# Optimization experiments

Measured on AMD Instinct MI355X. Metric: run time of the kernel, lower is better.

Reference implementation:

```python
import jax, jax.numpy as jnp
import numpy as np

EPS = 1e-12
LAMBDA = 0.5  # kernel['lambda'] for the binary kernel

D, H, Z = 3072, 1024, 32
BS, NN = 128, 32


def setup_inputs() -> dict:
    key = jax.random.key(0)
    ks = jax.random.split(key, 16)
    sc = lambda fan_in: 1.0 / np.sqrt(fan_in)
    inp = {
        "x_c": jax.random.normal(ks[0], (BS, D), jnp.float32),
        "x_nn": jax.random.normal(ks[1], (BS, NN, D), jnp.float32),
        # encoder params: D -> H -> H -> Z
        "We1": jax.random.normal(ks[2], (D, H), jnp.float32) * sc(D),
        "be1": jnp.zeros((H,), jnp.float32),
        "We2": jax.random.normal(ks[3], (H, H), jnp.float32) * sc(H),
        "be2": jnp.zeros((H,), jnp.float32),
        "We3": jax.random.normal(ks[4], (H, Z), jnp.float32) * sc(H),
        "be3": jnp.zeros((Z,), jnp.float32),
        # decoder params: Z -> H -> H -> D
        "Wd1": jax.random.normal(ks[5], (Z, H), jnp.float32) * sc(Z),
        "bd1": jnp.zeros((H,), jnp.float32),
        "Wd2": jax.random.normal(ks[6], (H, H), jnp.float32) * sc(H),
        "bd2": jnp.zeros((H,), jnp.float32),
        "Wd3": jax.random.normal(ks[7], (H, D), jnp.float32) * sc(H),
        "bd3": jnp.zeros((D,), jnp.float32),
    }
    return inp


def _mlp(x, W1, b1, W2, b2, W3, b3):
    h = jax.nn.relu(x @ W1 + b1)
    h = jax.nn.relu(h @ W2 + b2)
    return h @ W3 + b3


def reference(x_c, x_nn, We1, be1, We2, be2, We3, be3,
              Wd1, bd1, Wd2, bd2, Wd3, bd3):
    bs, num_nn, dim = x_nn.shape

    enc = lambda x: _mlp(x, We1, be1, We2, be2, We3, be3)
    dec = lambda z: _mlp(z, Wd1, bd1, Wd2, bd2, Wd3, bd3)

    z_c = enc(x_c)                                   # (bs, Z)
    z_dim = z_c.shape[1]
    z_nn = enc(x_nn.reshape(-1, dim)).reshape(bs, num_nn, z_dim)

    recon = dec(z_c)                                 # (bs, D)
    dz = z_nn - z_c[:, None, :]                      # (bs, nn, Z)
    v = dz.reshape(-1, z_dim)                        # (bs*nn, Z)
    inputs = jnp.broadcast_to(z_c[:, None, :], (bs, num_nn, z_dim)).reshape(-1, z_dim)

    # approx_order == 2: Jacobian-vector and Hessian-bilinear (dz^T H dz) via nested jvp
    jac_fn = lambda z: jax.jvp(dec, (z,), (v,))[1]   # J(z) dz, (bs*nn, D)
    jac, hess = jax.jvp(jac_fn, (inputs,), (v,))     # each (bs*nn, D)

    n_recon = recon[:, None, :] + (jac + 0.5 * hess).reshape(bs, num_nn, dim)

    n_loss = jnp.sum((x_nn - n_recon) ** 2, axis=2)  # ||.||^2, (bs, nn)

    # binary kernel: 1 where neighbor differs from center, lambda where identical
    dist = jnp.linalg.norm(x_c[:, None, :] - x_nn, axis=2)
    weights = jnp.where(dist > EPS, 1.0, LAMBDA)

    loss = jnp.mean(weights * n_loss)
    return loss
```

## Files before the change

### kernel.cpp

```cpp
#include <hip/hip_runtime.h>
#include <math.h>

#define D_DIM 3072
#define H_DIM 1024
#define Z_DIM 32
#define BATCH 128
#define NNEI 32
#define NROWS (BATCH * NNEI)
#define MENC (NROWS + BATCH)

typedef __attribute__((ext_vector_type(8))) short short8;
typedef __attribute__((ext_vector_type(4))) float f32x4;
typedef unsigned short ushortT;

__device__ __forceinline__ unsigned short f2bf(float f) {
  union { float f; unsigned int u; } v; v.f = f;
  unsigned int r = v.u + 0x7FFFu + ((v.u >> 16) & 1u);
  return (unsigned short)(r >> 16);
}
__device__ __forceinline__ float bf2f(unsigned short b) {
  union { unsigned int u; float f; } v; v.u = ((unsigned int)b) << 16;
  return v.f;
}

__device__ __forceinline__ void gl16(const ushortT* g, ushortT* l) {
  typedef __attribute__((address_space(1))) const void gvoid;
  typedef __attribute__((address_space(3))) void lvoid;
  __builtin_amdgcn_global_load_lds((gvoid*)(const void*)g, (lvoid*)(void*)l,
                                   16, 0, 0);
}
#define BAR() asm volatile("s_barrier" ::: "memory")
#define VM0() asm volatile("s_waitcnt vmcnt(0)" ::: "memory")

template <int N>
__device__ __forceinline__ void vmw() {
  if constexpr (N == 0)      asm volatile("s_waitcnt vmcnt(0)" ::: "memory");
  else if constexpr (N == 2) asm volatile("s_waitcnt vmcnt(2)" ::: "memory");
  else if constexpr (N == 3) asm volatile("s_waitcnt vmcnt(3)" ::: "memory");
  else if constexpr (N == 4) asm volatile("s_waitcnt vmcnt(4)" ::: "memory");
  else if constexpr (N == 6) asm volatile("s_waitcnt vmcnt(6)" ::: "memory");
  else if constexpr (N == 8) asm volatile("s_waitcnt vmcnt(8)" ::: "memory");
}

enum { EP_RELU = 0, EP_BIAS = 1, EP_PART = 2, EP_LOSS = 3 };

template <int MODE, int TN>
__global__ __launch_bounds__(256) __attribute__((amdgpu_waves_per_eu(2)))
void gemm32(
    const ushortT* __restrict__ A, const ushortT* __restrict__ BT,
    const float* __restrict__ bias, ushortT* __restrict__ C,
    float* __restrict__ P, int M, int N, int K, int Ks,
    const ushortT* __restrict__ xa,
    const float* __restrict__ wrow,
    float* __restrict__ out) {
  constexpr int NF = TN / 32;

  __shared__ __align__(16) ushortT As[4][4096];
  __shared__ __align__(16) ushortT Bs[4][TN * 32];

  const int t = threadIdx.x;
  const int wave = t >> 6;
  const int lane = t & 63;
  const int quad = lane >> 4;
  const int lm = lane & 15;

  int id = blockIdx.y * gridDim.x + blockIdx.x;
  const int nwg = gridDim.x * gridDim.y;
  if ((nwg & 7) == 0) id = (id & 7) * (nwg >> 3) + (id >> 3);
  const int bm = (id / gridDim.x) * 128;
  const int bn = (id % gridDim.x) * TN;

  const int koff = blockIdx.z * Ks;
  const int wr = (wave >> 1) * 64;
  const int wc = (wave & 1) * (TN / 2);

  f32x4 acc[4][NF];
#pragma unroll
  for (int i = 0; i < 4; ++i)
#pragma unroll
    for (int j = 0; j < NF; ++j) acc[i][j] = (f32x4)0.f;

  const int srow = lane & 15;
  const int skq = lane >> 4;
  const ushortT* gA =
      A + (size_t)(bm + wave * 32 + srow) * K + koff + skq * 8;
  const size_t row16 = (size_t)16 * K;

  const ushortT* gB;
  if (TN == 128) {
    gB = BT + (size_t)(bn + wave * 32 + srow) * K + koff + skq * 8;
  } else if (TN == 64) {
    gB = BT + (size_t)(bn + wave * 16 + srow) * K + koff + skq * 8;
  } else {
    gB = BT + (size_t)(bn + (wave & 1) * 16 + srow) * K + koff + skq * 8;
  }

#define STAGE(kk, sl)                                           \
  {                                                             \
    const size_t o = (size_t)(kk) * 32;                         \
    ushortT* lA = &As[sl][wave * 1024];                         \
    gl16(gA + o, lA);                                           \
    gl16(gA + row16 + o, lA + 512);                             \
    if (TN == 128) {                                            \
      ushortT* lB = &Bs[sl][wave * 1024];                       \
      gl16(gB + o, lB);                                         \
      gl16(gB + row16 + o, lB + 512);                           \
    } else if (TN == 64) {                                      \
      gl16(gB + o, &Bs[sl][wave * 512]);                        \
    } else {                                                    \
      if (wave < 2) gl16(gB + o, &Bs[sl][(wave & 1) * 512]);    \
    }                                                           \
  }

  const int nk = Ks / 32;
  for (int p = 0; p < 3 && p < nk; ++p) STAGE(p, p);

  for (int t0 = 0; t0 < nk; ++t0) {
    const int sl = t0 & 3;
    const int ahead = nk - 1 - t0;
    const int a2 = ahead >= 2 ? 2 : ahead;
    if (TN == 128) {
      if (a2 == 2) vmw<8>(); else if (a2 == 1) vmw<4>(); else vmw<0>();
    } else if (TN == 64) {
      if (a2 == 2) vmw<6>(); else if (a2 == 1) vmw<3>(); else vmw<0>();
    } else {
      if (wave < 2) {
        if (a2 == 2) vmw<6>(); else if (a2 == 1) vmw<3>(); else vmw<0>();
      } else {
        if (a2 == 2) vmw<4>(); else if (a2 == 1) vmw<2>(); else vmw<0>();
      }
    }
    BAR();
    if (t0 + 3 < nk) STAGE(t0 + 3, (t0 + 3) & 3);

    const ushortT* arp = &As[sl][(wr >> 4) * 512 + lane * 8];
    const ushortT* brp = &Bs[sl][(wc >> 4) * 512 + lane * 8];
    short8 af[4], bf[NF];
#pragma unroll
    for (int mt = 0; mt < 4; ++mt) af[mt] = *(const short8*)(arp + mt * 512);
#pragma unroll
    for (int nt = 0; nt < NF; ++nt) bf[nt] = *(const short8*)(brp + nt * 512);
#pragma unroll
    for (int mt = 0; mt < 4; ++mt)
#pragma unroll
      for (int nt = 0; nt < NF; ++nt)
        acc[mt][nt] = __builtin_amdgcn_mfma_f32_16x16x32_bf16(
            af[mt], bf[nt], acc[mt][nt], 0, 0, 0);
  }
#undef STAGE

  if (MODE == EP_LOSS) {
    __shared__ float red[256];
    float lsum = 0.f;
#pragma unroll
    for (int mt = 0; mt < 4; ++mt) {
#pragma unroll
      for (int r = 0; r < 4; ++r) {
        const int row = bm + wr + mt * 16 + quad * 4 + r;
        const float w = wrow[row];
        const ushortT* xr = xa + (size_t)row * N;
        float rs = 0.f;
#pragma unroll
        for (int nt = 0; nt < NF; ++nt) {
          const int col = bn + wc + nt * 16 + lm;
          const float d = bf2f(xr[col]) - (acc[mt][nt][r] + bias[col]);
          rs = fmaf(d, d, rs);
        }
        lsum = fmaf(w, rs, lsum);
      }
    }
    __syncthreads();
    red[t] = lsum;
    __syncthreads();
    for (int st = 128; st > 0; st >>= 1) {
      if (t < st) red[t] += red[t + st];
      __syncthreads();
    }
    if (t == 0) atomicAdd(out, red[0] * (1.0f / (float)NROWS));
  } else if (MODE == EP_PART) {
#pragma unroll
    for (int mt = 0; mt < 4; ++mt)
#pragma unroll
      for (int r = 0; r < 4; ++r) {
        const int row = bm + wr + mt * 16 + quad * 4 + r;
#pragma unroll
        for (int nt = 0; nt < NF; ++nt) {
          const int col = bn + wc + nt * 16 + lm;
          P[((size_t)blockIdx.z * M + row) * N + col] = acc[mt][nt][r];
        }
      }
  } else {
#pragma unroll
    for (int mt = 0; mt < 4; ++mt)
#pragma unroll
      for (int r = 0; r < 4; ++r) {
        const int row = bm + wr + mt * 16 + quad * 4 + r;
#pragma unroll
        for (int nt = 0; nt < NF; ++nt) {
          const int col = bn + wc + nt * 16 + lm;
          float v = acc[mt][nt][r] + bias[col];
          if (MODE == EP_RELU) v = fmaxf(v, 0.f);
          C[(size_t)row * N + col] = f2bf(v);
        }
      }
  }
}

template <int MODE, int TN>
__global__ __launch_bounds__(256) void gemm_sb(
    const ushortT* __restrict__ A, const ushortT* __restrict__ BT,
    const float* __restrict__ bias, ushortT* __restrict__ C,
    int M, int N, int K,
    const ushortT* __restrict__ xa, const float* __restrict__ wrow,
    float* __restrict__ out) {
  constexpr int NF = TN / 32;
  __shared__ __align__(16) ushortT As[4096];
  __shared__ __align__(16) ushortT Bs[TN * 32];

  const int t = threadIdx.x;
  const int wave = t >> 6;
  const int lane = t & 63;
  const int quad = lane >> 4;
  const int lm = lane & 15;

  int id = blockIdx.y * gridDim.x + blockIdx.x;
  const int nwg = gridDim.x * gridDim.y;
  if ((nwg & 7) == 0) id = (id & 7) * (nwg >> 3) + (id >> 3);
  const int bm = (id / gridDim.x) * 128;
  const int bn = (id % gridDim.x) * TN;

  const int wr = (wave >> 1) * 64;
  const int wc = (wave & 1) * (TN / 2);

  const int a_r0 = (t >> 6) * 16 + (t & 15);
  const int a_q8 = ((t >> 4) & 3) * 8;
  const ushortT* ga0 = A + (size_t)(bm + a_r0) * K + a_q8;
  const ushortT* gb0 = BT + (size_t)(bn + a_r0) * K + a_q8;

  ushortT* asw = &As[wave * 512];
  ushortT* bsw = &Bs[wave * 512];
  gl16(ga0, asw);
  gl16(ga0 + (size_t)64 * K, asw + 2048);
  gl16(gb0, bsw);
  if (TN == 128) gl16(gb0 + (size_t)64 * K, bsw + 2048);
  VM0();
  BAR();

  f32x4 acc[4][NF];
#pragma unroll
  for (int i = 0; i < 4; ++i)
#pragma unroll
    for (int j = 0; j < NF; ++j) acc[i][j] = (f32x4)0.f;

  const ushortT* arp = As + (wr >> 4) * 512 + lane * 8;
  const ushortT* brp = Bs + (wc >> 4) * 512 + lane * 8;
  short8 af[4], bf[NF];
#pragma unroll
  for (int mt = 0; mt < 4; ++mt) af[mt] = *(const short8*)(arp + mt * 512);
#pragma unroll
  for (int nt = 0; nt < NF; ++nt) bf[nt] = *(const short8*)(brp + nt * 512);
#pragma unroll
  for (int mt = 0; mt < 4; ++mt)
#pragma unroll
    for (int nt = 0; nt < NF; ++nt)
      acc[mt][nt] = __builtin_amdgcn_mfma_f32_16x16x32_bf16(
          af[mt], bf[nt], acc[mt][nt], 0, 0, 0);

#pragma unroll
  for (int mt = 0; mt < 4; ++mt)
#pragma unroll
    for (int r = 0; r < 4; ++r) {
      const int row = bm + wr + mt * 16 + quad * 4 + r;
#pragma unroll
      for (int nt = 0; nt < NF; ++nt) {
        const int col = bn + wc + nt * 16 + lm;
        float v = acc[mt][nt][r] + bias[col];
        if (MODE == EP_RELU) v = fmaxf(v, 0.f);
        C[(size_t)row * N + col] = f2bf(v);
      }
    }
}

template <int S, int RELU>
__global__ __launch_bounds__(256) void reduce_lin(
    const float* __restrict__ P, const float* __restrict__ bias,
    ushortT* __restrict__ outp, int MN, int Nmask) {
  const int i4 = (blockIdx.x * 256 + threadIdx.x) * 4;
  if (i4 >= MN) return;
  float4 s = *(const float4*)(P + i4);
#pragma unroll
  for (int k = 1; k < S; ++k) {
    const float4 q = *(const float4*)(P + (size_t)k * MN + i4);
    s.x += q.x; s.y += q.y; s.z += q.z; s.w += q.w;
  }
  const float4 b = *(const float4*)(bias + (i4 & Nmask));
  float vx = s.x + b.x, vy = s.y + b.y, vz = s.z + b.z, vw = s.w + b.w;
  if (RELU) {
    vx = fmaxf(vx, 0.f); vy = fmaxf(vy, 0.f);
    vz = fmaxf(vz, 0.f); vw = fmaxf(vw, 0.f);
  }
  ushort4 o;
  o.x = f2bf(vx); o.y = f2bf(vy); o.z = f2bf(vz); o.w = f2bf(vw);
  *(ushort4*)(outp + i4) = o;
}

__global__ __launch_bounds__(256) void mask_apply(
    const ushortT* __restrict__ U, ushortT* __restrict__ outp) {
  const int i4 = (blockIdx.x * 256 + threadIdx.x) * 4;
  const int r = i4 >> 10;
  const int c = i4 & 1023;
  ushort4 u = *(const ushort4*)(U + i4);
  ushort4 o;
  if (r < NROWS) {
    const ushort4 m = *(const ushort4*)(U + (((size_t)(NROWS + (r >> 5))) << 10) + c);
    o.x = ((short)m.x > 0) ? u.x : 0;
    o.y = ((short)m.y > 0) ? u.y : 0;
    o.z = ((short)m.z > 0) ? u.z : 0;
    o.w = ((short)m.w > 0) ? u.w : 0;
  } else {
    o.x = ((short)u.x > 0) ? u.x : 0;
    o.y = ((short)u.y > 0) ? u.y : 0;
    o.z = ((short)u.z > 0) ? u.z : 0;
    o.w = ((short)u.w > 0) ? u.w : 0;
  }
  *(ushort4*)(outp + i4) = o;
}

__global__ __launch_bounds__(256) void prep_kernel(
    const float* __restrict__ x_c, const float* __restrict__ x_nn,
    ushortT* __restrict__ A_enc, float* __restrict__ wbuf, float* __restrict__ out) {
  const int i = blockIdx.x;
  const int t = threadIdx.x;
  if (i < NROWS) {
    const float* src = x_nn + (size_t)i * D_DIM;
    const float* ctr = x_c + (size_t)(i >> 5) * D_DIM;
    ushortT* dst = A_enc + (size_t)i * D_DIM;
    float s = 0.f;
    for (int d = t * 4; d < D_DIM; d += 1024) {
      const float4 v = *(const float4*)(src + d);
      const float4 c = *(const float4*)(ctr + d);
      ushort4 o;
      o.x = f2bf(v.x); o.y = f2bf(v.y); o.z = f2bf(v.z); o.w = f2bf(v.w);
      *(ushort4*)(dst + d) = o;
      const float dx = v.x - c.x, dy = v.y - c.y, dz = v.z - c.z, dw = v.w - c.w;
      s += dx * dx + dy * dy + dz * dz + dw * dw;
    }
    __shared__ float red[256];
    red[t] = s;
    __syncthreads();
    for (int st = 128; st > 0; st >>= 1) {
      if (t < st) red[t] += red[t + st];
      __syncthreads();
    }
    if (t == 0) {
      wbuf[i] = (red[0] > 1e-24f) ? 1.0f : 0.5f;
      if (i == 0) out[0] = 0.f;
    }
  } else {
    const int r = i - NROWS;
    const float* src = x_c + (size_t)r * D_DIM;
    ushortT* dst = A_enc + (size_t)i * D_DIM;
    for (int d = t * 4; d < D_DIM; d += 1024) {
      const float4 v = *(const float4*)(src + d);
      ushort4 o;
      o.x = f2bf(v.x); o.y = f2bf(v.y); o.z = f2bf(v.z); o.w = f2bf(v.w);
      *(ushort4*)(dst + d) = o;
    }
  }
}

__global__ __launch_bounds__(256) void trans_all(
    const float* __restrict__ We1, const float* __restrict__ We2,
    const float* __restrict__ We3, const float* __restrict__ Wd1,
    const float* __restrict__ Wd2, const float* __restrict__ Wd3,
    ushortT* __restrict__ We1T, ushortT* __restrict__ We2T,
    ushortT* __restrict__ We3T, ushortT* __restrict__ Wd1T,
    ushortT* __restrict__ Wd2T, ushortT* __restrict__ Wd3T) {
  const int b = blockIdx.x;
  const float* W; ushortT* WT; int K, N, loc;
  if (b < 3072)      { W = We1; WT = We1T; K = 3072; N = 1024; loc = b; }
  else if (b < 4096) { W = We2; WT = We2T; K = 1024; N = 1024; loc = b - 3072; }
  else if (b < 4128) { W = We3; WT = We3T; K = 1024; N = 32;   loc = b - 4096; }
  else if (b < 4160) { W = Wd1; WT = Wd1T; K = 32;   N = 1024; loc = b - 4128; }
  else if (b < 5184) { W = Wd2; WT = Wd2T; K = 1024; N = 1024; loc = b - 4160; }
  else               { W = Wd3; WT = Wd3T; K = 1024; N = 3072; loc = b - 5184; }
  const int ntiles = N >> 5;
  const int n0 = (loc % ntiles) * 32;
  const int k0 = (loc / ntiles) * 32;
  __shared__ float tile[32][33];
  const int tx = threadIdx.x & 31;
  const int ty = threadIdx.x >> 5;
  for (int i = ty; i < 32; i += 8)
    tile[i][tx] = W[(size_t)(k0 + i) * N + n0 + tx];
  __syncthreads();
  for (int i = ty; i < 32; i += 8)
    WT[(size_t)(n0 + i) * K + k0 + tx] = f2bf(tile[tx][i]);
}

extern "C" void kernel_launch(void* const* d_in, const int* in_sizes, int n_in,
                              void* d_out, int out_size, void* d_ws, size_t ws_size,
                              hipStream_t stream) {
  const float* x_c = (const float*)d_in[0];
  const float* x_nn = (const float*)d_in[1];
  const float* We1 = (const float*)d_in[2];
  const float* be1 = (const float*)d_in[3];
  const float* We2 = (const float*)d_in[4];
  const float* be2 = (const float*)d_in[5];
  const float* We3 = (const float*)d_in[6];
  const float* be3 = (const float*)d_in[7];
  const float* Wd1 = (const float*)d_in[8];
  const float* bd1 = (const float*)d_in[9];
  const float* Wd2 = (const float*)d_in[10];
  const float* bd2 = (const float*)d_in[11];
  const float* Wd3 = (const float*)d_in[12];
  const float* bd3 = (const float*)d_in[13];
  float* out = (float*)d_out;

  char* p = (char*)d_ws;
  auto alloc = [&](size_t bytes) {
    char* r = p;
    p += (bytes + 255) & ~(size_t)255;
    return r;
  };
  ushortT* We1T = (ushortT*)alloc((size_t)H_DIM * D_DIM * 2);
  ushortT* We2T = (ushortT*)alloc((size_t)H_DIM * H_DIM * 2);
  ushortT* We3T = (ushortT*)alloc((size_t)Z_DIM * H_DIM * 2);
  ushortT* Wd1T = (ushortT*)alloc((size_t)H_DIM * Z_DIM * 2);
  ushortT* Wd2T = (ushortT*)alloc((size_t)H_DIM * H_DIM * 2);
  ushortT* Wd3T = (ushortT*)alloc((size_t)D_DIM * H_DIM * 2);
  ushortT* A_enc = (ushortT*)alloc((size_t)MENC * D_DIM * 2);
  ushortT* bufX = (ushortT*)alloc((size_t)MENC * H_DIM * 2);
  ushortT* bufY = (ushortT*)alloc((size_t)MENC * H_DIM * 2);
  ushortT* z = (ushortT*)alloc((size_t)MENC * Z_DIM * 2);
  float* Pbig = (float*)alloc((size_t)3 * MENC * H_DIM * 4);
  float* wbuf = (float*)alloc((size_t)NROWS * 4);

  const dim3 blk(256);
  const float* nofp = nullptr;
  const ushortT* nobf = nullptr;

  prep_kernel<<<dim3(MENC), blk, 0, stream>>>(x_c, x_nn, A_enc, wbuf, out);
  trans_all<<<dim3(8256), blk, 0, stream>>>(We1, We2, We3, Wd1, Wd2, Wd3,
                                            We1T, We2T, We3T, Wd1T, Wd2T, Wd3T);

  gemm32<EP_PART, 128><<<dim3(8, 33, 3), blk, 0, stream>>>(
      A_enc, We1T, nofp, nullptr, Pbig, MENC, H_DIM, D_DIM, D_DIM / 3,
      nobf, nofp, nullptr);
  reduce_lin<3, 1><<<dim3((MENC * H_DIM) / 1024), blk, 0, stream>>>(
      Pbig, be1, bufX, MENC * H_DIM, H_DIM - 1);

  gemm32<EP_PART, 128><<<dim3(8, 33, 2), blk, 0, stream>>>(
      bufX, We2T, nofp, nullptr, Pbig, MENC, H_DIM, H_DIM, H_DIM / 2,
      nobf, nofp, nullptr);
  reduce_lin<2, 1><<<dim3((MENC * H_DIM) / 1024), blk, 0, stream>>>(
      Pbig, be2, bufY, MENC * H_DIM, H_DIM - 1);

  gemm32<EP_PART, 32><<<dim3(1, 33, 8), blk, 0, stream>>>(
      bufY, We3T, nofp, nullptr, Pbig, MENC, Z_DIM, H_DIM, H_DIM / 8,
      nobf, nofp, nullptr);
  reduce_lin<8, 0><<<dim3((MENC * Z_DIM) / 1024), blk, 0, stream>>>(
      Pbig, be3, z, MENC * Z_DIM, Z_DIM - 1);

  gemm_sb<EP_BIAS, 64><<<dim3(16, 33), blk, 0, stream>>>(
      z, Wd1T, bd1, bufX, MENC, H_DIM, Z_DIM, nobf, nofp, nullptr);
  mask_apply<<<dim3((MENC * H_DIM) / 1024), blk, 0, stream>>>(bufX, bufY);
  gemm32<EP_PART, 128><<<dim3(8, 33, 2), blk, 0, stream>>>(
      bufY, Wd2T, nofp, nullptr, Pbig, MENC, H_DIM, H_DIM, H_DIM / 2,
      nobf, nofp, nullptr);
  reduce_lin<2, 0><<<dim3((MENC * H_DIM) / 1024), blk, 0, stream>>>(
      Pbig, bd2, bufX, MENC * H_DIM, H_DIM - 1);
  mask_apply<<<dim3((NROWS * H_DIM) / 1024), blk, 0, stream>>>(bufX, bufY);
  gemm32<EP_LOSS, 128><<<dim3(24, 32, 1), blk, 0, stream>>>(
      bufY, Wd3T, bd3, nullptr, nullptr, NROWS, D_DIM, H_DIM, H_DIM,
      A_enc, wbuf, out);
}
```

Before: 405.7 us.

## Use three-stage LDS pipeline, raise occupancy hint, and use inline-asm LDS reads

Shrinks the GEMM's shared-memory ring from four stages to three, so loads are issued two tiles ahead instead of three, and raises the waves-per-EU hint from 2 to 3. The aim is to fit more waves per CU and hide latency through occupancy rather than pipeline depth. The LDS fragment loads become explicit ds_read_b128 inline asm followed by an lgkmcnt wait and a scheduling barrier, which gives a fixed instruction order before the MFMAs. The cost is a shallower prefetch window, a possible register cap from the occupancy hint, and less freedom for the compiler to overlap LDS reads with the MFMAs.

```diff
diff --git a/kernel.cpp b/kernel.cpp
--- a/kernel.cpp
+++ b/kernel.cpp
@@ -29,8 +29,17 @@
   __builtin_amdgcn_global_load_lds((gvoid*)(const void*)g, (lvoid*)(void*)l,
                                    16, 0, 0);
 }
+
+typedef __attribute__((address_space(3))) const ushortT lds_cus;
+__device__ __forceinline__ short8 ldsr(const ushortT* p) {
+  short8 r;
+  asm volatile("ds_read_b128 %0, %1" : "=v"(r) : "v"((lds_cus*)p));
+  return r;
+}
+
 #define BAR() asm volatile("s_barrier" ::: "memory")
 #define VM0() asm volatile("s_waitcnt vmcnt(0)" ::: "memory")
+#define LGKM0() asm volatile("s_waitcnt lgkmcnt(0)" ::: "memory")
 
 template <int N>
 __device__ __forceinline__ void vmw() {
@@ -38,14 +47,12 @@
   else if constexpr (N == 2) asm volatile("s_waitcnt vmcnt(2)" ::: "memory");
   else if constexpr (N == 3) asm volatile("s_waitcnt vmcnt(3)" ::: "memory");
   else if constexpr (N == 4) asm volatile("s_waitcnt vmcnt(4)" ::: "memory");
-  else if constexpr (N == 6) asm volatile("s_waitcnt vmcnt(6)" ::: "memory");
-  else if constexpr (N == 8) asm volatile("s_waitcnt vmcnt(8)" ::: "memory");
 }
 
 enum { EP_RELU = 0, EP_BIAS = 1, EP_PART = 2, EP_LOSS = 3 };
 
 template <int MODE, int TN>
-__global__ __launch_bounds__(256) __attribute__((amdgpu_waves_per_eu(2)))
+__global__ __launch_bounds__(256) __attribute__((amdgpu_waves_per_eu(3)))
 void gemm32(
     const ushortT* __restrict__ A, const ushortT* __restrict__ BT,
     const float* __restrict__ bias, ushortT* __restrict__ C,
@@ -55,8 +62,8 @@
     float* __restrict__ out) {
   constexpr int NF = TN / 32;
 
-  __shared__ __align__(16) ushortT As[4][4096];
-  __shared__ __align__(16) ushortT Bs[4][TN * 32];
+  __shared__ __align__(16) ushortT As[3][4096];
+  __shared__ __align__(16) ushortT Bs[3][TN * 32];
 
   const int t = threadIdx.x;
   const int wave = t >> 6;
@@ -113,39 +120,40 @@
   }
 
   const int nk = Ks / 32;
-  for (int p = 0; p < 3 && p < nk; ++p) STAGE(p, p);
-
+  STAGE(0, 0);
+  if (nk > 1) STAGE(1, 1);
+
+  int sl = 0;
+  int sn = 2;
   for (int t0 = 0; t0 < nk; ++t0) {
-    const int sl = t0 & 3;
-    const int ahead = nk - 1 - t0;
-    const int a2 = ahead >= 2 ? 2 : ahead;
-    if (TN == 128) {
-      if (a2 == 2) vmw<8>(); else if (a2 == 1) vmw<4>(); else vmw<0>();
-    } else if (TN == 64) {
-      if (a2 == 2) vmw<6>(); else if (a2 == 1) vmw<3>(); else vmw<0>();
+    if (t0 + 1 < nk) {
+      if (TN == 128) vmw<4>();
+      else if (TN == 64) vmw<3>();
+      else { if (wave < 2) vmw<3>(); else vmw<2>(); }
     } else {
-      if (wave < 2) {
-        if (a2 == 2) vmw<6>(); else if (a2 == 1) vmw<3>(); else vmw<0>();
-      } else {
-        if (a2 == 2) vmw<4>(); else if (a2 == 1) vmw<2>(); else vmw<0>();
-      }
+      vmw<0>();
     }
     BAR();
-    if (t0 + 3 < nk) STAGE(t0 + 3, (t0 + 3) & 3);
+    if (t0 + 2 < nk) STAGE(t0 + 2, sn);
 
     const ushortT* arp = &As[sl][(wr >> 4) * 512 + lane * 8];
     const ushortT* brp = &Bs[sl][(wc >> 4) * 512 + lane * 8];
     short8 af[4], bf[NF];
 #pragma unroll
-    for (int mt = 0; mt < 4; ++mt) af[mt] = *(const short8*)(arp + mt * 512);
-#pragma unroll
-    for (int nt = 0; nt < NF; ++nt) bf[nt] = *(const short8*)(brp + nt * 512);
+    for (int mt = 0; mt < 4; ++mt) af[mt] = ldsr(arp + mt * 512);
+#pragma unroll
+    for (int nt = 0; nt < NF; ++nt) bf[nt] = ldsr(brp + nt * 512);
+    LGKM0();
+    __builtin_amdgcn_sched_barrier(0);
 #pragma unroll
     for (int mt = 0; mt < 4; ++mt)
 #pragma unroll
       for (int nt = 0; nt < NF; ++nt)
         acc[mt][nt] = __builtin_amdgcn_mfma_f32_16x16x32_bf16(
             af[mt], bf[nt], acc[mt][nt], 0, 0, 0);
+
+    sl = (sl == 2) ? 0 : sl + 1;
+    sn = (sn == 2) ? 0 : sn + 1;
   }
 #undef STAGE
 
@@ -256,9 +264,11 @@
   const ushortT* brp = Bs + (wc >> 4) * 512 + lane * 8;
   short8 af[4], bf[NF];
 #pragma unroll
-  for (int mt = 0; mt < 4; ++mt) af[mt] = *(const short8*)(arp + mt * 512);
-#pragma unroll
-  for (int nt = 0; nt < NF; ++nt) bf[nt] = *(const short8*)(brp + nt * 512);
+  for (int mt = 0; mt < 4; ++mt) af[mt] = ldsr(arp + mt * 512);
+#pragma unroll
+  for (int nt = 0; nt < NF; ++nt) bf[nt] = ldsr(brp + nt * 512);
+  LGKM0();
+  __builtin_amdgcn_sched_barrier(0);
 #pragma unroll
   for (int mt = 0; mt < 4; ++mt)
 #pragma unroll
```

Measured after the change: 368.9 us. 9.1% less time.
